# Kernel tuning notes

Measured on AMD Instinct MI355X. Metric: run time of the kernel, lower is better.

The kernel has to match this reference:

```python
import jax, jax.numpy as jnp
import numpy as np

CHUNK = 64


def _rmsnorm(x, g, eps=1e-6):
    return x * jax.lax.rsqrt(jnp.mean(x * x, axis=-1, keepdims=True) + eps) * g


def setup_inputs() -> dict:
    key = jax.random.key(0)
    ks = jax.random.split(key, 8)
    B, L, D, N = 4, 4096, 512, 64
    s = 0.02
    return {
        'x': jax.random.normal(ks[0], (B, L, D), jnp.float32),
        'A_log': -jnp.ones((D,), jnp.float32) * jnp.log(2.0),
        'dt_bias': jnp.log(jnp.expm1(jax.random.uniform(ks[1], (D,), jnp.float32, 0.001, 0.1))),
        'D_skip': jnp.ones((D,), jnp.float32),
        'W_xproj': jax.random.normal(ks[2], (D, 2 * D), jnp.float32) * s,
        'b_xproj': jnp.zeros((2 * D,), jnp.float32),
        'W_B': jax.random.normal(ks[3], (D, N), jnp.float32) * s,
        'W_C': jax.random.normal(ks[4], (D, N), jnp.float32) * s,
        'W_dt': jax.random.normal(ks[5], (D, D), jnp.float32) * s,
        'g_Bnorm': jnp.ones((N,), jnp.float32),
        'g_Cnorm': jnp.ones((N,), jnp.float32),
        'g_outnorm': jnp.ones((D,), jnp.float32),
        'W_out': jax.random.normal(ks[6], (D, D), jnp.float32) * s,
        'b_out': jnp.zeros((D,), jnp.float32),
    }


def reference(x, A_log, dt_bias, D_skip, W_xproj, b_xproj, W_B, W_C, W_dt,
              g_Bnorm, g_Cnorm, g_outnorm, W_out, b_out):
    b, l, d = x.shape
    n = W_B.shape[1]
    p = CHUNK
    c = l // p  # L chosen divisible by chunk size (original pads otherwise)

    A = -jnp.exp(jnp.clip(A_log, -20.0, 2.0))  # (d,)
    xp = x @ W_xproj + b_xproj                  # (b,l,2d)
    x_bar, z = jnp.split(xp, 2, axis=-1)
    Bm = _rmsnorm(x_bar @ W_B, g_Bnorm)         # (b,l,n)
    Cm = _rmsnorm(x_bar @ W_C, g_Cnorm)         # (b,l,n)
    dt = jnp.clip(jax.nn.softplus(x_bar @ W_dt + dt_bias), 1e-4, 5.0)
    A_bar = jnp.exp(jnp.clip(dt * A, -20.0, 0.0))  # (b,l,d)

    to_chunks = lambda t: t.reshape(b, c, p, t.shape[-1]).transpose(1, 0, 2, 3)
    xc, Bc, Cc, Ac = map(to_chunks, (x_bar, Bm, Cm, A_bar))  # (c,b,p,*)
    mask = jnp.tril(jnp.ones((p, p), x.dtype))

    def process_chunk(prev_state, inputs):
        x_c, B_c, C_c, A_c = inputs
        log_a = jnp.log(jnp.clip(A_c, 1e-8, 1.0))
        la_cs = jnp.cumsum(log_a, axis=1)  # (b,p,d)
        # intra-chunk decay matrix M: (b,p,p,d)
        M = jnp.exp(la_cs[:, :, None, :] - la_cs[:, None, :, :]) * mask[None, :, :, None]
        BX = jnp.einsum('bpn,bpd->bpnd', B_c, x_c)
        state = jnp.einsum('bijd,bjnd->bind', M, BX)
        y_intra = jnp.einsum('bpn,bpnd->bpd', C_c, state)
        decay = jnp.exp(la_cs)
        y_inter = jnp.einsum('bpn,bpnd->bpd', C_c,
                             prev_state[:, None, :, :] * decay[:, :, None, :])
        y_c = y_intra + y_inter
        a_total = jnp.exp(la_cs[:, -1, :])             # (b,d)
        a_to_end = jnp.exp(la_cs[:, -1:, :] - la_cs)   # (b,p,d)
        chunk_state = jnp.einsum('bpn,bpd->bnd', B_c, x_c * a_to_end)
        new_state = prev_state * a_total[:, None, :] + chunk_state
        new_state = jnp.where(jnp.isfinite(new_state), new_state, 0.0)
        y_c = jnp.where(jnp.isfinite(y_c), y_c, 0.0)
        return new_state, y_c

    init = jnp.zeros((b, n, d), x.dtype)
    _, yc = jax.lax.scan(jax.checkpoint(process_chunk), init, (xc, Bc, Cc, Ac))
    y = yc.transpose(1, 0, 2, 3).reshape(b, l, d)
    y = jnp.where(jnp.isfinite(y), y, 0.0)
    y = y + D_skip * x_bar
    y = _rmsnorm(y, g_outnorm) * jax.nn.silu(z)
    return y @ W_out + b_out
```

## Files before the change

kernel.cpp:

```cpp
#include <hip/hip_runtime.h>
#include <hip/hip_bf16.h>
#include <math.h>

typedef __hip_bfloat16 bf16;
typedef __attribute__((ext_vector_type(8))) short short8;
typedef __attribute__((ext_vector_type(4))) float floatx4;
typedef __attribute__((ext_vector_type(2))) float floatx2;

#define B_ 4
#define L_ 4096
#define D_ 512
#define M_ (B_*L_)

__device__ __forceinline__ float b2f(bf16 v){ return __bfloat162float(v); }
__device__ __forceinline__ bf16  f2b(float v){ return __float2bfloat16(v); }
__device__ __forceinline__ short f2bs(float v){ bf16 h = __float2bfloat16(v); short s; __builtin_memcpy(&s,&h,2); return s; }
__device__ __forceinline__ floatx2 fx2(float v){ floatx2 r; r.x=v; r.y=v; return r; }

#define GLD16(gp, lp) __builtin_amdgcn_global_load_lds( \
    (const __attribute__((address_space(1))) void*)(gp), \
    (__attribute__((address_space(3))) void*)(lp), 16, 0, 0)

__global__ __launch_bounds__(1024) void k_transpose(const float* __restrict__ src,
                                                    bf16* __restrict__ dst, int K, int N){
    __shared__ float tile[32][33];
    int n0 = blockIdx.x*32, k0 = blockIdx.y*32;
    int tx = threadIdx.x, ty = threadIdx.y;
    tile[ty][tx] = src[(size_t)(k0+ty)*N + n0+tx];
    __syncthreads();
    ((short*)dst)[(size_t)(n0+ty)*K + k0+tx] = f2bs(tile[tx][ty]);
}

__global__ __launch_bounds__(256) void k_cvt(const float* __restrict__ src,
                                             bf16* __restrict__ dst){
    size_t i = ((size_t)blockIdx.x*256 + threadIdx.x)*4;
    float4 v = *(const float4*)(src + i);
    short4 s; s.x=f2bs(v.x); s.y=f2bs(v.y); s.z=f2bs(v.z); s.w=f2bs(v.w);
    *(short4*)((short*)dst + i) = s;
}

template<int EPI>
__global__ __launch_bounds__(256) void k_gemm(const bf16* __restrict__ Ap,
        const bf16* __restrict__ Wt, const float* __restrict__ bias,
        const float* __restrict__ aux,
        float* __restrict__ o1, bf16* __restrict__ o2, bf16* __restrict__ o3,
        float* __restrict__ o4){
    __shared__ short As[128*32];
    __shared__ short Bs[128*32];
    const int K = 512;
    int m0 = blockIdx.x*128, n0 = blockIdx.y*128;
    int tid=threadIdx.x, w=tid>>6, lane=tid&63;
    int wr=w>>1, wc=w&1, quad=lane>>4, r16=lane&15;
    floatx4 acc[4][4];
    #pragma unroll
    for (int i=0;i<4;i++)
        #pragma unroll
        for (int j=0;j<4;j++)
            #pragma unroll
            for (int e=0;e<4;e++) acc[i][j][e]=0.f;

    int c0 = tid, c1 = tid + 256;
    const short* Ab = (const short*)Ap + (size_t)m0*K;
    const short* Wb = (const short*)Wt + (size_t)n0*K;
    int r0 = c0>>2, g0 = (c0&3)*8;
    int r1 = c1>>2, g1 = (c1&3)*8;

    for (int k0=0;k0<K;k0+=32){
        GLD16(Ab + (size_t)r0*K + k0 + g0, &As[c0*8]);
        GLD16(Ab + (size_t)r1*K + k0 + g1, &As[c1*8]);
        GLD16(Wb + (size_t)r0*K + k0 + g0, &Bs[c0*8]);
        GLD16(Wb + (size_t)r1*K + k0 + g1, &Bs[c1*8]);
        __syncthreads();
        short8 af[4], bv[4];
        #pragma unroll
        for (int i=0;i<4;i++) af[i] = *(short8*)&As[(wr*64+i*16+r16)*32 + quad*8];
        #pragma unroll
        for (int j=0;j<4;j++) bv[j] = *(short8*)&Bs[(wc*64+j*16+r16)*32 + quad*8];
        #pragma unroll
        for (int i=0;i<4;i++)
            #pragma unroll
            for (int j=0;j<4;j++)
                acc[i][j] = __builtin_amdgcn_mfma_f32_16x16x32_bf16(af[i], bv[j], acc[i][j], 0,0,0);
        __syncthreads();
    }
    if (EPI==3){
        #pragma unroll
        for (int i=0;i<4;i++)
        #pragma unroll
        for (int reg=0;reg<4;reg++){
            float ss=0.f;
            #pragma unroll
            for (int j=0;j<4;j++){ float t=acc[i][j][reg]; ss+=t*t; }
            #pragma unroll
            for (int m=1;m<16;m<<=1) ss += __shfl_xor(ss, m, 64);
            float rq = rsqrtf(ss*(1.f/64.f)+1e-6f);
            int gr = m0 + wr*64 + i*16 + quad*4 + reg;
            #pragma unroll
            for (int j=0;j<4;j++){
                int gc = wc*64 + j*16 + r16;
                float gval = (gc<64) ? bias[gc] : aux[gc-64];
                float v = acc[i][j][reg]*rq*gval;
                if (gc<64) o1[(size_t)gr*64 + gc] = v;
                else       o4[(size_t)gr*64 + (gc-64)] = v;
            }
        }
        return;
    }
    #pragma unroll
    for (int i=0;i<4;i++)
    #pragma unroll
    for (int j=0;j<4;j++)
    #pragma unroll
    for (int reg=0;reg<4;reg++){
        int gr = m0 + wr*64 + i*16 + quad*4 + reg;
        int gc = n0 + wc*64 + j*16 + r16;
        float v = acc[i][j][reg] + bias[gc];
        if (EPI==0){
            if (gc < 512){
                o1[(size_t)gr*512 + gc] = v;
                o2[(size_t)gr*512 + gc] = f2b(v);
            } else {
                o3[(size_t)gr*512 + (gc-512)] = f2b(v / (1.f + __expf(-v)));
            }
        } else if (EPI==1){
            float sp = (v > 15.f) ? v : log1pf(__expf(v));
            float dt = fminf(fmaxf(sp, 1e-4f), 5.f);
            float Ad = -__expf(fminf(fmaxf(aux[gc], -20.f), 2.f));
            o1[(size_t)gr*512 + gc] = fminf(fmaxf(dt*Ad, -18.420680743952367f), 0.f);
        } else {
            o1[(size_t)gr*512 + gc] = v;
        }
    }
}

__global__ __launch_bounds__(256) void k_pass1(const float* __restrict__ la,
        const float* __restrict__ xbar, const float* __restrict__ Bm,
        float* __restrict__ local, float* __restrict__ atot){
    __shared__ float Bs[64*64];
    int c=blockIdx.x, b=blockIdx.y;
    int d = threadIdx.x*2;
    size_t rowbase=(size_t)b*L_+(size_t)c*64;
    size_t cb=(size_t)c*4+b;
    {
        const float4* src=(const float4*)(Bm + rowbase*64);
        float4* dst=(float4*)Bs;
        #pragma unroll
        for (int k=0;k<4;k++) dst[k*256+threadIdx.x]=src[k*256+threadIdx.x];
    }
    __syncthreads();
    floatx2 st[64];
    #pragma unroll
    for (int n=0;n<64;n++) st[n]=fx2(0.f);
    floatx2 cs=fx2(0.f);
    size_t off0=rowbase*512+d;
    floatx2 la_n=*(const floatx2*)(la+off0), x_n=*(const floatx2*)(xbar+off0);
    #pragma unroll 2
    for (int i=0;i<64;i++){
        floatx2 lai=la_n, xi=x_n;
        if (i<63){ la_n=*(const floatx2*)(la+off0+(i+1)*512);
                   x_n =*(const floatx2*)(xbar+off0+(i+1)*512); }
        floatx2 ai; ai.x=__expf(lai.x); ai.y=__expf(lai.y);
        cs = cs + lai;
        const float* Br=Bs+i*64;
        #pragma unroll
        for (int k=0;k<16;k++){
            float4 bv=*(const float4*)(Br+k*4);
            st[k*4+0]=ai*st[k*4+0]+fx2(bv.x)*xi;
            st[k*4+1]=ai*st[k*4+1]+fx2(bv.y)*xi;
            st[k*4+2]=ai*st[k*4+2]+fx2(bv.z)*xi;
            st[k*4+3]=ai*st[k*4+3]+fx2(bv.w)*xi;
        }
    }
    #pragma unroll
    for (int n=0;n<64;n++)
        *(floatx2*)(local + (cb*64+n)*512 + d) = st[n];
    floatx2 at; at.x=__expf(cs.x); at.y=__expf(cs.y);
    *(floatx2*)(atot + cb*512 + d) = at;
}

__global__ __launch_bounds__(256) void k_scan(float* __restrict__ local,
        const float* __restrict__ atot){
    int idx = blockIdx.x*256 + threadIdx.x;
    int d = idx & 511, n = (idx >> 9) & 63, b = idx >> 15;
    float s = 0.f;
    for (int c=0;c<64;c++){
        size_t cb = (size_t)c*4 + b;
        size_t off = (cb*64 + n)*512 + d;
        float v = local[off];
        local[off] = s;
        s = s * atot[cb*512 + d] + v;
        if (!isfinite(s)) s = 0.f;
    }
}

__global__ __launch_bounds__(256) void k_pass2(const float* __restrict__ la,
        const float* __restrict__ xbar, const float* __restrict__ Bm,
        const float* __restrict__ Cm, const float* __restrict__ Sprev,
        float* __restrict__ ybuf){
    __shared__ float Bs[64*64];
    __shared__ float Cs[64*64];
    int c=blockIdx.x, b=blockIdx.y;
    int d = threadIdx.x*2;
    size_t rowbase=(size_t)b*L_+(size_t)c*64;
    size_t cb=(size_t)c*4+b;
    {
        const float4* sb=(const float4*)(Bm + rowbase*64);
        const float4* sc=(const float4*)(Cm + rowbase*64);
        float4* db=(float4*)Bs; float4* dc=(float4*)Cs;
        #pragma unroll
        for (int k=0;k<4;k++){
            db[k*256+threadIdx.x]=sb[k*256+threadIdx.x];
            dc[k*256+threadIdx.x]=sc[k*256+threadIdx.x];
        }
    }
    floatx2 st[64];
    #pragma unroll
    for (int n=0;n<64;n++)
        st[n] = *(const floatx2*)(Sprev + (cb*64+n)*512 + d);
    __syncthreads();
    size_t off0=rowbase*512+d;
    floatx2 la_n=*(const floatx2*)(la+off0), x_n=*(const floatx2*)(xbar+off0);
    #pragma unroll 2
    for (int i=0;i<64;i++){
        floatx2 lai=la_n, xi=x_n;
        if (i<63){ la_n=*(const floatx2*)(la+off0+(i+1)*512);
                   x_n =*(const floatx2*)(xbar+off0+(i+1)*512); }
        floatx2 ai; ai.x=__expf(lai.x); ai.y=__expf(lai.y);
        const float* Br=Bs+i*64;
        const float* Cr=Cs+i*64;
        floatx2 yv=fx2(0.f);
        #pragma unroll
        for (int k=0;k<16;k++){
            float4 bv=*(const float4*)(Br+k*4);
            float4 cv=*(const float4*)(Cr+k*4);
            floatx2 s;
            s=ai*st[k*4+0]+fx2(bv.x)*xi; st[k*4+0]=s; yv=yv+fx2(cv.x)*s;
            s=ai*st[k*4+1]+fx2(bv.y)*xi; st[k*4+1]=s; yv=yv+fx2(cv.y)*s;
            s=ai*st[k*4+2]+fx2(bv.z)*xi; st[k*4+2]=s; yv=yv+fx2(cv.z)*s;
            s=ai*st[k*4+3]+fx2(bv.w)*xi; st[k*4+3]=s; yv=yv+fx2(cv.w)*s;
        }
        if (!isfinite(yv.x)) yv.x=0.f;
        if (!isfinite(yv.y)) yv.y=0.f;
        *(floatx2*)(ybuf + off0 + (size_t)i*512) = yv;
    }
}

__global__ __launch_bounds__(256) void k_outnorm(const float* __restrict__ y,
        const float* __restrict__ xbar, const float* __restrict__ Dskip,
        const float* __restrict__ g, const bf16* __restrict__ siluz,
        bf16* __restrict__ u){
    int wave = threadIdx.x >> 6, lane = threadIdx.x & 63;
    size_t row = (size_t)blockIdx.x*4 + wave;
    float v[8]; float ss = 0.f;
    #pragma unroll
    for (int j=0;j<8;j++){
        int d = j*64 + lane;
        float t = y[row*512 + d] + Dskip[d] * xbar[row*512 + d];
        v[j] = t; ss += t*t;
    }
    #pragma unroll
    for (int m=1;m<64;m<<=1) ss += __shfl_xor(ss, m, 64);
    float r = rsqrtf(ss*(1.f/512.f) + 1e-6f);
    #pragma unroll
    for (int j=0;j<8;j++){
        int d = j*64 + lane;
        u[row*512 + d] = f2b(v[j] * r * g[d] * b2f(siluz[row*512 + d]));
    }
}

extern "C" void kernel_launch(void* const* d_in, const int* in_sizes, int n_in,
                              void* d_out, int out_size, void* d_ws, size_t ws_size,
                              hipStream_t stream){
    const float* x       = (const float*)d_in[0];
    const float* A_log   = (const float*)d_in[1];
    const float* dt_bias = (const float*)d_in[2];
    const float* D_skip  = (const float*)d_in[3];
    const float* W_xproj = (const float*)d_in[4];
    const float* b_xproj = (const float*)d_in[5];
    const float* W_B     = (const float*)d_in[6];
    const float* W_C     = (const float*)d_in[7];
    const float* W_dt    = (const float*)d_in[8];
    const float* g_B     = (const float*)d_in[9];
    const float* g_C     = (const float*)d_in[10];
    const float* g_out   = (const float*)d_in[11];
    const float* W_out   = (const float*)d_in[12];
    const float* b_out   = (const float*)d_in[13];
    float* out = (float*)d_out;

    char* wp = (char*)d_ws;
    auto alloc = [&](size_t bytes)->char*{ char* p = wp; wp += (bytes + 255) & ~(size_t)255; return p; };
    float* xbar  = (float*)alloc((size_t)M_*512*4);
    bf16*  xh    = (bf16*) alloc((size_t)M_*512*2);
    bf16*  xbarh = (bf16*) alloc((size_t)M_*512*2);
    bf16*  siluz = (bf16*) alloc((size_t)M_*512*2);
    float* la    = (float*)alloc((size_t)M_*512*4);
    float* Bm    = (float*)alloc((size_t)M_*64*4);
    float* Cm    = (float*)alloc((size_t)M_*64*4);
    float* local = (float*)alloc((size_t)256*64*512*4);
    float* atot  = (float*)alloc((size_t)256*512*4);
    float* ybuf  = (float*)alloc((size_t)M_*512*4);
    bf16*  u     = (bf16*) alloc((size_t)M_*512*2);
    bf16*  WtX   = (bf16*) alloc((size_t)1024*512*2);
    bf16*  WtD   = (bf16*) alloc((size_t)512*512*2);
    bf16*  WtO   = (bf16*) alloc((size_t)512*512*2);
    bf16*  WtBC  = (bf16*) alloc((size_t)128*512*2);

    dim3 tb(32,32);
    k_transpose<<<dim3(32,16), tb, 0, stream>>>(W_xproj, WtX, 512, 1024);
    k_transpose<<<dim3(16,16), tb, 0, stream>>>(W_dt,   WtD, 512, 512);
    k_transpose<<<dim3(16,16), tb, 0, stream>>>(W_out,  WtO, 512, 512);
    k_transpose<<<dim3(2,16),  tb, 0, stream>>>(W_B,    WtBC,          512, 64);
    k_transpose<<<dim3(2,16),  tb, 0, stream>>>(W_C,    WtBC+64*512,   512, 64);
    k_cvt      <<<M_*512/1024, 256, 0, stream>>>(x, xh);

    k_gemm<0> <<<dim3(128, 8), 256, 0, stream>>>(xh,    WtX,  b_xproj, nullptr, xbar, xbarh, siluz, nullptr);
    k_gemm<3> <<<dim3(128, 1), 256, 0, stream>>>(xbarh, WtBC, g_B, g_C, Bm, nullptr, nullptr, Cm);
    k_gemm<1> <<<dim3(128, 4), 256, 0, stream>>>(xbarh, WtD,  dt_bias, A_log, la, nullptr, nullptr, nullptr);
    k_pass1   <<<dim3(64, 4),  256, 0, stream>>>(la, xbar, Bm, local, atot);
    k_scan    <<<512,          256, 0, stream>>>(local, atot);
    k_pass2   <<<dim3(64, 4),  256, 0, stream>>>(la, xbar, Bm, Cm, local, ybuf);
    k_outnorm <<<M_/4,         256, 0, stream>>>(ybuf, xbar, D_skip, g_out, siluz, u);
    k_gemm<2> <<<dim3(128, 4), 256, 0, stream>>>(u,     WtO,  b_out, nullptr, out, nullptr, nullptr, nullptr);
}
```

Before: 375.5 us.

## Split scan state dimension across two blocks and store chunk states in bf16

The pass1/pass2 chunked-scan kernels now split the 64-wide state dimension into two halves over a third grid axis. This doubles the block count from 256, which was barely one block per CU, and halves per-thread state registers. The inter-chunk local states are stored and scanned in bf16 with two elements per thread, cutting that traffic. pass2 writes two partial y buffers that outnorm sums, with the non-finite check moved there. The trade-offs are extra y write/read traffic, duplicated la/xbar reads and exp work per half, and reduced precision of the carried states.

Result: faster. 355.1 us (-5.4%).

```diff
diff --git a/kernel.cpp b/kernel.cpp
--- a/kernel.cpp
+++ b/kernel.cpp
@@ -15,6 +15,8 @@
 __device__ __forceinline__ float b2f(bf16 v){ return __bfloat162float(v); }
 __device__ __forceinline__ bf16  f2b(float v){ return __float2bfloat16(v); }
 __device__ __forceinline__ short f2bs(float v){ bf16 h = __float2bfloat16(v); short s; __builtin_memcpy(&s,&h,2); return s; }
+__device__ __forceinline__ unsigned short f2bus(float v){ bf16 h = __float2bfloat16(v); unsigned short s; __builtin_memcpy(&s,&h,2); return s; }
+__device__ __forceinline__ float bus2f(unsigned short u){ unsigned int x = ((unsigned int)u)<<16; float f; __builtin_memcpy(&f,&x,4); return f; }
 __device__ __forceinline__ floatx2 fx2(float v){ floatx2 r; r.x=v; r.y=v; return r; }
 
 #define GLD16(gp, lp) __builtin_amdgcn_global_load_lds( \
@@ -135,22 +137,22 @@
 
 __global__ __launch_bounds__(256) void k_pass1(const float* __restrict__ la,
         const float* __restrict__ xbar, const float* __restrict__ Bm,
-        float* __restrict__ local, float* __restrict__ atot){
-    __shared__ float Bs[64*64];
-    int c=blockIdx.x, b=blockIdx.y;
+        unsigned short* __restrict__ localh, float* __restrict__ atot){
+    __shared__ float Bs[64*32];
+    int c=blockIdx.x, b=blockIdx.y, nh=blockIdx.z;
     int d = threadIdx.x*2;
     size_t rowbase=(size_t)b*L_+(size_t)c*64;
     size_t cb=(size_t)c*4+b;
-    {
-        const float4* src=(const float4*)(Bm + rowbase*64);
-        float4* dst=(float4*)Bs;
-        #pragma unroll
-        for (int k=0;k<4;k++) dst[k*256+threadIdx.x]=src[k*256+threadIdx.x];
+    #pragma unroll
+    for (int it=0;it<2;it++){
+        int idx=it*256+threadIdx.x;
+        int row=idx>>3, grp=idx&7;
+        *(float4*)&Bs[row*32+grp*4] = *(const float4*)(Bm + (rowbase+row)*64 + nh*32 + grp*4);
     }
     __syncthreads();
-    floatx2 st[64];
-    #pragma unroll
-    for (int n=0;n<64;n++) st[n]=fx2(0.f);
+    floatx2 st[32];
+    #pragma unroll
+    for (int n=0;n<32;n++) st[n]=fx2(0.f);
     floatx2 cs=fx2(0.f);
     size_t off0=rowbase*512+d;
     floatx2 la_n=*(const floatx2*)(la+off0), x_n=*(const floatx2*)(xbar+off0);
@@ -161,9 +163,9 @@
                    x_n =*(const floatx2*)(xbar+off0+(i+1)*512); }
         floatx2 ai; ai.x=__expf(lai.x); ai.y=__expf(lai.y);
         cs = cs + lai;
-        const float* Br=Bs+i*64;
-        #pragma unroll
-        for (int k=0;k<16;k++){
+        const float* Br=Bs+i*32;
+        #pragma unroll
+        for (int k=0;k<8;k++){
             float4 bv=*(const float4*)(Br+k*4);
             st[k*4+0]=ai*st[k*4+0]+fx2(bv.x)*xi;
             st[k*4+1]=ai*st[k*4+1]+fx2(bv.y)*xi;
@@ -172,53 +174,61 @@
         }
     }
     #pragma unroll
-    for (int n=0;n<64;n++)
-        *(floatx2*)(local + (cb*64+n)*512 + d) = st[n];
-    floatx2 at; at.x=__expf(cs.x); at.y=__expf(cs.y);
-    *(floatx2*)(atot + cb*512 + d) = at;
-}
-
-__global__ __launch_bounds__(256) void k_scan(float* __restrict__ local,
+    for (int n=0;n<32;n++){
+        ushort2 p; p.x=f2bus(st[n].x); p.y=f2bus(st[n].y);
+        *(ushort2*)(localh + (cb*64 + nh*32 + n)*512 + d) = p;
+    }
+    if (nh==0){
+        floatx2 at; at.x=__expf(cs.x); at.y=__expf(cs.y);
+        *(floatx2*)(atot + cb*512 + d) = at;
+    }
+}
+
+__global__ __launch_bounds__(256) void k_scan(unsigned short* __restrict__ localh,
         const float* __restrict__ atot){
     int idx = blockIdx.x*256 + threadIdx.x;
-    int d = idx & 511, n = (idx >> 9) & 63, b = idx >> 15;
-    float s = 0.f;
+    int d = (idx & 255)*2, n = (idx >> 8) & 63, b = idx >> 14;
+    float sx=0.f, sy=0.f;
     for (int c=0;c<64;c++){
         size_t cb = (size_t)c*4 + b;
         size_t off = (cb*64 + n)*512 + d;
-        float v = local[off];
-        local[off] = s;
-        s = s * atot[cb*512 + d] + v;
-        if (!isfinite(s)) s = 0.f;
+        ushort2 v = *(ushort2*)(localh+off);
+        float vx=bus2f(v.x), vy=bus2f(v.y);
+        ushort2 wp; wp.x=f2bus(sx); wp.y=f2bus(sy);
+        *(ushort2*)(localh+off) = wp;
+        float2 at = *(const float2*)(atot + cb*512 + d);
+        sx = sx*at.x + vx; sy = sy*at.y + vy;
+        if (!isfinite(sx)) sx = 0.f;
+        if (!isfinite(sy)) sy = 0.f;
     }
 }
 
 __global__ __launch_bounds__(256) void k_pass2(const float* __restrict__ la,
         const float* __restrict__ xbar, const float* __restrict__ Bm,
-        const float* __restrict__ Cm, const float* __restrict__ Sprev,
+        const float* __restrict__ Cm, const unsigned short* __restrict__ Sprevh,
         float* __restrict__ ybuf){
-    __shared__ float Bs[64*64];
-    __shared__ float Cs[64*64];
-    int c=blockIdx.x, b=blockIdx.y;
+    __shared__ float Bs[64*32];
+    __shared__ float Cs[64*32];
+    int c=blockIdx.x, b=blockIdx.y, nh=blockIdx.z;
     int d = threadIdx.x*2;
     size_t rowbase=(size_t)b*L_+(size_t)c*64;
     size_t cb=(size_t)c*4+b;
-    {
-        const float4* sb=(const float4*)(Bm + rowbase*64);
-        const float4* sc=(const float4*)(Cm + rowbase*64);
-        float4* db=(float4*)Bs; float4* dc=(float4*)Cs;
-        #pragma unroll
-        for (int k=0;k<4;k++){
-            db[k*256+threadIdx.x]=sb[k*256+threadIdx.x];
-            dc[k*256+threadIdx.x]=sc[k*256+threadIdx.x];
-        }
-    }
-    floatx2 st[64];
-    #pragma unroll
-    for (int n=0;n<64;n++)
-        st[n] = *(const floatx2*)(Sprev + (cb*64+n)*512 + d);
+    #pragma unroll
+    for (int it=0;it<2;it++){
+        int idx=it*256+threadIdx.x;
+        int row=idx>>3, grp=idx&7;
+        *(float4*)&Bs[row*32+grp*4] = *(const float4*)(Bm + (rowbase+row)*64 + nh*32 + grp*4);
+        *(float4*)&Cs[row*32+grp*4] = *(const float4*)(Cm + (rowbase+row)*64 + nh*32 + grp*4);
+    }
+    floatx2 st[32];
+    #pragma unroll
+    for (int n=0;n<32;n++){
+        ushort2 p = *(const ushort2*)(Sprevh + (cb*64 + nh*32 + n)*512 + d);
+        st[n].x = bus2f(p.x); st[n].y = bus2f(p.y);
+    }
     __syncthreads();
     size_t off0=rowbase*512+d;
+    float* yout = ybuf + (size_t)nh*M_*512;
     floatx2 la_n=*(const floatx2*)(la+off0), x_n=*(const floatx2*)(xbar+off0);
     #pragma unroll 2
     for (int i=0;i<64;i++){
@@ -226,11 +236,11 @@
         if (i<63){ la_n=*(const floatx2*)(la+off0+(i+1)*512);
                    x_n =*(const floatx2*)(xbar+off0+(i+1)*512); }
         floatx2 ai; ai.x=__expf(lai.x); ai.y=__expf(lai.y);
-        const float* Br=Bs+i*64;
-        const float* Cr=Cs+i*64;
+        const float* Br=Bs+i*32;
+        const float* Cr=Cs+i*32;
         floatx2 yv=fx2(0.f);
         #pragma unroll
-        for (int k=0;k<16;k++){
+        for (int k=0;k<8;k++){
             float4 bv=*(const float4*)(Br+k*4);
             float4 cv=*(const float4*)(Cr+k*4);
             floatx2 s;
@@ -239,13 +249,12 @@
             s=ai*st[k*4+2]+fx2(bv.z)*xi; st[k*4+2]=s; yv=yv+fx2(cv.z)*s;
             s=ai*st[k*4+3]+fx2(bv.w)*xi; st[k*4+3]=s; yv=yv+fx2(cv.w)*s;
         }
-        if (!isfinite(yv.x)) yv.x=0.f;
-        if (!isfinite(yv.y)) yv.y=0.f;
-        *(floatx2*)(ybuf + off0 + (size_t)i*512) = yv;
-    }
-}
-
-__global__ __launch_bounds__(256) void k_outnorm(const float* __restrict__ y,
+        *(floatx2*)(yout + off0 + (size_t)i*512) = yv;
+    }
+}
+
+__global__ __launch_bounds__(256) void k_outnorm(const float* __restrict__ yA,
+        const float* __restrict__ yB,
         const float* __restrict__ xbar, const float* __restrict__ Dskip,
         const float* __restrict__ g, const bf16* __restrict__ siluz,
         bf16* __restrict__ u){
@@ -255,7 +264,9 @@
     #pragma unroll
     for (int j=0;j<8;j++){
         int d = j*64 + lane;
-        float t = y[row*512 + d] + Dskip[d] * xbar[row*512 + d];
+        float yv = yA[row*512 + d] + yB[row*512 + d];
+        if (!isfinite(yv)) yv = 0.f;
+        float t = yv + Dskip[d] * xbar[row*512 + d];
         v[j] = t; ss += t*t;
     }
     #pragma unroll
@@ -296,9 +307,9 @@
     float* la    = (float*)alloc((size_t)M_*512*4);
     float* Bm    = (float*)alloc((size_t)M_*64*4);
     float* Cm    = (float*)alloc((size_t)M_*64*4);
-    float* local = (float*)alloc((size_t)256*64*512*4);
+    unsigned short* localh = (unsigned short*)alloc((size_t)256*64*512*2);
     float* atot  = (float*)alloc((size_t)256*512*4);
-    float* ybuf  = (float*)alloc((size_t)M_*512*4);
+    float* ybuf  = (float*)alloc((size_t)2*M_*512*4);
     bf16*  u     = (bf16*) alloc((size_t)M_*512*2);
     bf16*  WtX   = (bf16*) alloc((size_t)1024*512*2);
     bf16*  WtD   = (bf16*) alloc((size_t)512*512*2);
@@ -316,9 +327,9 @@
     k_gemm<0> <<<dim3(128, 8), 256, 0, stream>>>(xh,    WtX,  b_xproj, nullptr, xbar, xbarh, siluz, nullptr);
     k_gemm<3> <<<dim3(128, 1), 256, 0, stream>>>(xbarh, WtBC, g_B, g_C, Bm, nullptr, nullptr, Cm);
     k_gemm<1> <<<dim3(128, 4), 256, 0, stream>>>(xbarh, WtD,  dt_bias, A_log, la, nullptr, nullptr, nullptr);
-    k_pass1   <<<dim3(64, 4),  256, 0, stream>>>(la, xbar, Bm, local, atot);
-    k_scan    <<<512,          256, 0, stream>>>(local, atot);
-    k_pass2   <<<dim3(64, 4),  256, 0, stream>>>(la, xbar, Bm, Cm, local, ybuf);
-    k_outnorm <<<M_/4,         256, 0, stream>>>(ybuf, xbar, D_skip, g_out, siluz, u);
+    k_pass1   <<<dim3(64,4,2), 256, 0, stream>>>(la, xbar, Bm, localh, atot);
+    k_scan    <<<256,          256, 0, stream>>>(localh, atot);
+    k_pass2   <<<dim3(64,4,2), 256, 0, stream>>>(la, xbar, Bm, Cm, localh, ybuf);
+    k_outnorm <<<M_/4,         256, 0, stream>>>(ybuf, ybuf+(size_t)M_*512, xbar, D_skip, g_out, siluz, u);
     k_gemm<2> <<<dim3(128, 4), 256, 0, stream>>>(u,     WtO,  b_out, nullptr, out, nullptr, nullptr, nullptr);
 }
```
